# Optimization experiments

Hardware: AMD Instinct MI355X
Metric: run time of the kernel (lower is better)

Reference implementation:

```python
import jax, jax.numpy as jnp
import numpy as np

B, C, F, T = 4, 64, 64, 128
IC = 32  # inter_channels = C // 2
EPS = 1e-5  # BatchNorm eps


def _conv1x1(x, w, b=None):
    # x: (B, Cin, H, W), w: (Cout, Cin)
    y = jnp.einsum('bchw,oc->bohw', x, w)
    if b is not None:
        y = y + b[None, :, None, None]
    return y


def _maxpool2(x):
    b, c, h, w = x.shape
    return x.reshape(b, c, h // 2, 2, w // 2, 2).max(axis=(3, 5))


def _pos_score(fsz, tsz, h2_w):
    # positional encoding is (fpos, tpos) in [0,1]; the 2->1 conv head makes the
    # pos_delta contribution separable: score(n,m) = s(n) - s(m)
    fpos = jnp.linspace(0.0, 1.0, fsz)
    tpos = jnp.linspace(0.0, 1.0, tsz)
    return (h2_w[0] * fpos[:, None] + h2_w[1] * tpos[None, :]).reshape(-1)


def setup_inputs() -> dict:
    key = jax.random.key(0)
    ks = jax.random.split(key, 16)
    s = 0.05
    inp = {
        'x': jax.random.normal(ks[0], (B, C, F, T), dtype=jnp.float32),
        'psi_w': jax.random.normal(ks[1], (IC, C)) * s,
        'psi_b': jax.random.normal(ks[2], (IC,)) * s,
        'theta_w': jax.random.normal(ks[3], (IC, C)) * s,
        'theta_b': jax.random.normal(ks[4], (IC,)) * s,
        'phi_w': jax.random.normal(ks[5], (IC, C)) * s,
        'phi_b': jax.random.normal(ks[6], (IC,)) * s,
        'h0_w': jax.random.normal(ks[7], (IC,)) * s,
        'h1_w': jax.random.normal(ks[8], (IC,)) * s,
        'h2_w': jax.random.normal(ks[9], (2,)) * s,
        'W_w': jax.random.normal(ks[10], (C, IC + 1)) * s,
        'W_b': jax.random.normal(ks[11], (C,)) * s,
        'bn_gamma': jax.random.normal(ks[12], (C,)) * s + 1.0,
        'bn_beta': jax.random.normal(ks[13], (C,)) * s,
        'bn_mean': jax.random.normal(ks[14], (C,)) * s,
        'bn_var': jax.random.uniform(ks[15], (C,), minval=0.5, maxval=1.5),
    }
    return inp


def reference(x, psi_w, psi_b, theta_w, theta_b, phi_w, phi_b,
              h0_w, h1_w, h2_w, W_w, W_b, bn_gamma, bn_beta, bn_mean, bn_var):
    Bs, Cs, Fs, Ts = x.shape
    N = Fs * Ts
    M = (Fs // 2) * (Ts // 2)

    psi_x = _maxpool2(_conv1x1(x, psi_w, psi_b))      # (B, IC, F/2, T/2)
    theta_x = _conv1x1(x, theta_w, theta_b)           # (B, IC, F, T)
    phi_x = _maxpool2(_conv1x1(x, phi_w, phi_b))      # (B, IC, F/2, T/2)

    # additive attention scores: relu(head0(theta) + head1(phi) + head2(pos_delta))
    t_score = jnp.einsum('bcft,c->bft', theta_x, h0_w).reshape(Bs, N)   # (B, N)
    p_score = jnp.einsum('bcft,c->bft', phi_x, h1_w).reshape(Bs, M)     # (B, M)
    a = _pos_score(Fs, Ts, h2_w)             # (N,) query pos contribution
    bpos = _pos_score(Fs // 2, Ts // 2, h2_w)  # (M,) key pos contribution
    f = jax.nn.relu((t_score + a[None, :])[:, :, None]
                    + (p_score - bpos[None, :])[:, None, :])  # (B, N, M)

    f_div = f / jnp.asarray(M, f.dtype)
    psi_flat = psi_x.reshape(Bs, IC, M)
    y = jnp.einsum('bnm,bcm->bcn', f_div, psi_flat).reshape(Bs, IC, Fs, Ts)

    # r_structure_type='zero' -> structure feature is zeros (1 extra channel)
    structure = jnp.zeros((Bs, 1, Fs, Ts), dtype=y.dtype)
    y = jnp.concatenate([y, structure], axis=1)       # (B, IC+1, F, T)

    wy = _conv1x1(y, W_w, W_b)                        # (B, C, F, T)
    inv = bn_gamma / jnp.sqrt(bn_var + EPS)
    wy = wy * inv[None, :, None, None] + (bn_beta - bn_mean * inv)[None, :, None, None]
    return wy + x
```

## Files before the change

### kernel.cpp

```cpp
#include <hip/hip_runtime.h>

#define B_ 4
#define C_ 64
#define F_ 64
#define T_ 128
#define IC_ 32
#define N_ 8192
#define M_ 2048

#define OFF_U      0
#define OFF_PSI2   32768
#define OFF_V      294912
#define OFF_VS     303104
#define OFF_Q01    311296
#define WS_FLOATS  1360384

__device__ __align__(16) float g_ws[WS_FLOATS];
__device__ int g_perm[B_ * M_];

__global__ __launch_bounds__(256) void k1(
    const float* __restrict__ x,
    const float* __restrict__ psi_w, const float* __restrict__ psi_b,
    const float* __restrict__ theta_w, const float* __restrict__ theta_b,
    const float* __restrict__ phi_w, const float* __restrict__ phi_b,
    const float* __restrict__ h0_w, const float* __restrict__ h1_w,
    const float* __restrict__ h2_w)
{
    float* __restrict__ ws = g_ws;
    __shared__ __align__(16) float xs[4096];
    __shared__ __align__(16) float pw[2048];
    __shared__ __align__(16) float fw[2048];
    __shared__ float wt_l[64];

    const int tid = threadIdx.x;
    const int bid = blockIdx.x;
    const int b = bid >> 7;
    const int rem = bid & 127;
    const int fh = rem >> 2;
    const int q = rem & 3;
    const int c0 = q * 32;

    for (int idx = tid; idx < 1024; idx += 256) {
        const int c = idx >> 4, r2 = (idx >> 3) & 1, t4 = idx & 7;
        const float4 v = *(const float4*)&x[(((size_t)b * 64 + c) * 64 + (2 * fh + r2)) * 128 + c0 + 4 * t4];
        *(float4*)&xs[c * 64 + r2 * 32 + 4 * t4] = v;
    }
    for (int idx = tid; idx < 2048; idx += 256) {
        const int c4 = idx >> 7, o = (idx >> 2) & 31, j = idx & 3;
        pw[idx] = psi_w[o * 64 + 4 * c4 + j];
        fw[idx] = phi_w[o * 64 + 4 * c4 + j];
    }
    if (tid < 64) {
        float acc = 0.f;
        for (int o2 = 0; o2 < 32; ++o2)
            acc += h0_w[o2] * theta_w[o2 * 64 + tid];
        wt_l[tid] = acc;
    }
    __syncthreads();

    const float h20 = h2_w[0], h21 = h2_w[1];

    {
        const int o = tid & 31, g = tid >> 5;
        const float pb = psi_b[o], fb = phi_b[o], h1 = h1_w[o];
        const float4* pw4 = (const float4*)pw;
        const float4* fw4 = (const float4*)fw;
        const float4* xs4 = (const float4*)xs;
        float sp[2][4] = {{0,0,0,0},{0,0,0,0}};
        float sf[2][4] = {{0,0,0,0},{0,0,0,0}};
        for (int c4 = 0; c4 < 16; ++c4) {
            const float4 pv = pw4[c4 * 32 + o];
            const float4 fv = fw4[c4 * 32 + o];
            const float* pvf = (const float*)&pv;
            const float* fvf = (const float*)&fv;
#pragma unroll
            for (int j = 0; j < 4; ++j) {
                const int c = 4 * c4 + j;
                const float4 r0 = xs4[c * 16 + g];
                const float4 r1 = xs4[c * 16 + 8 + g];
                const float wp = pvf[j], wf = fvf[j];
                sp[0][0] += wp * r0.x; sp[0][1] += wp * r0.y;
                sp[0][2] += wp * r1.x; sp[0][3] += wp * r1.y;
                sp[1][0] += wp * r0.z; sp[1][1] += wp * r0.w;
                sp[1][2] += wp * r1.z; sp[1][3] += wp * r1.w;
                sf[0][0] += wf * r0.x; sf[0][1] += wf * r0.y;
                sf[0][2] += wf * r1.x; sf[0][3] += wf * r1.y;
                sf[1][0] += wf * r0.z; sf[1][1] += wf * r0.w;
                sf[1][2] += wf * r1.z; sf[1][3] += wf * r1.w;
            }
        }
#pragma unroll
        for (int h = 0; h < 2; ++h) {
            const int hc = 2 * g + h;
            const float psiv = fmaxf(fmaxf(sp[h][0], sp[h][1]), fmaxf(sp[h][2], sp[h][3])) + pb;
            const float phiv = fmaxf(fmaxf(sf[h][0], sf[h][1]), fmaxf(sf[h][2], sf[h][3])) + fb;
            const int m = fh * 64 + q * 16 + hc;
            ws[OFF_PSI2 + ((size_t)b * 2048 + m) * 32 + o] = psiv;
            float tv = h1 * phiv;
            for (int mask = 1; mask < 32; mask <<= 1)
                tv += __shfl_xor(tv, mask, 64);
            if (o == 0) {
                const float bpos = h20 * (fh * (1.0f / 31.0f))
                                 + h21 * ((q * 16 + hc) * (1.0f / 63.0f));
                ws[OFF_V + b * 2048 + m] = tv - bpos;
            }
        }
    }

    if (tid < 64) {
        const int r2 = tid >> 5, tl = tid & 31;
        float acc = 0.f;
        for (int c = 0; c < 64; ++c)
            acc += xs[c * 64 + r2 * 32 + tl] * wt_l[c];
        float tb_ = 0.f;
        for (int o2 = 0; o2 < 32; ++o2)
            tb_ += h0_w[o2] * theta_b[o2];
        const int f = 2 * fh + r2, tt = c0 + tl;
        const int n = f * 128 + tt;
        const float a = h20 * (f * (1.0f / 63.0f)) + h21 * (tt * (1.0f / 127.0f));
        ws[OFF_U + b * 8192 + n] = acc + tb_ + a;
    }
}

__global__ __launch_bounds__(256) void k2()
{
    float* __restrict__ ws = g_ws;
    __shared__ __align__(16) float vl[2048];
    __shared__ int part[256];
    const int tid = threadIdx.x;
    const int b = blockIdx.x >> 7, chunk = blockIdx.x & 127;
    const float* v = ws + OFF_V + b * 2048;
    for (int i = tid; i < 2048; i += 256) vl[i] = v[i];
    __syncthreads();

    const int ml = tid >> 4;
    const int jq = tid & 15;
    const int m = chunk * 16 + ml;
    const float vm = vl[m];
    int cnt = 0;
    const float4* v4 = (const float4*)vl;
#pragma unroll 4
    for (int i = 0; i < 32; ++i) {
        const int j4 = jq + 16 * i;
        const float4 vv = v4[j4];
        const int jb = j4 * 4;
        cnt += (vv.x > vm) || (vv.x == vm && (jb    ) < m);
        cnt += (vv.y > vm) || (vv.y == vm && (jb + 1) < m);
        cnt += (vv.z > vm) || (vv.z == vm && (jb + 2) < m);
        cnt += (vv.w > vm) || (vv.w == vm && (jb + 3) < m);
    }
    part[tid] = cnt;
    __syncthreads();
    if (tid < 16) {
        int r = 0;
#pragma unroll
        for (int j = 0; j < 16; ++j) r += part[tid * 16 + j];
        ws[OFF_VS + b * 2048 + r] = vl[chunk * 16 + tid];
        g_perm[b * 2048 + r] = chunk * 16 + tid;
    }
}

__global__ __launch_bounds__(512) void k3(const float* __restrict__ W_w)
{
    float* __restrict__ ws = g_ws;
    __shared__ float Wrow[32];
    __shared__ float wt0[8], wt1[8];
    const int tid = threadIdx.x;
    const int b = blockIdx.x >> 6, o = blockIdx.x & 63;
    if (tid < 32) Wrow[tid] = W_w[o * 33 + tid];
    __syncthreads();

    const int* perm = g_perm + b * 2048;
    const float* vs = ws + OFF_VS + b * 2048;
    const float* psi2 = ws + OFF_PSI2 + (size_t)b * 2048 * 32;

    float zl[4], vlv[4];
    float s0 = 0.f, s1 = 0.f;
    const int base = tid * 4;
#pragma unroll
    for (int qq = 0; qq < 4; ++qq) {
        const int i = base + qq;
        const int mp = perm[i];
        const float4* pr = (const float4*)(psi2 + (size_t)mp * 32);
        float z = 0.f;
#pragma unroll
        for (int w = 0; w < 8; ++w) {
            const float4 p4 = pr[w];
            z += Wrow[4 * w] * p4.x + Wrow[4 * w + 1] * p4.y
               + Wrow[4 * w + 2] * p4.z + Wrow[4 * w + 3] * p4.w;
        }
        const float vv = vs[i];
        zl[qq] = z; vlv[qq] = vv;
        s0 += z; s1 += vv * z;
    }

    float w0 = s0, w1 = s1;
    const int lane = tid & 63, wv = tid >> 6;
#pragma unroll
    for (int off = 1; off < 64; off <<= 1) {
        const float t0_ = __shfl_up(w0, off, 64);
        const float t1_ = __shfl_up(w1, off, 64);
        if (lane >= off) { w0 += t0_; w1 += t1_; }
    }
    if (lane == 63) { wt0[wv] = w0; wt1[wv] = w1; }
    __syncthreads();
    float base0 = 0.f, base1 = 0.f;
    for (int w = 0; w < wv; ++w) { base0 += wt0[w]; base1 += wt1[w]; }
    float r0 = w0 + base0 - s0, r1 = w1 + base1 - s1;

    float2* Q01 = (float2*)(ws + OFF_Q01) + (size_t)b * 2049 * 64;
#pragma unroll
    for (int qq = 0; qq < 4; ++qq) {
        r0 += zl[qq]; r1 += vlv[qq] * zl[qq];
        float2 p; p.x = r0; p.y = r1;
        Q01[(size_t)(base + qq + 1) * 64 + o] = p;
    }
    if (tid == 0) { float2 z2; z2.x = 0.f; z2.y = 0.f; Q01[o] = z2; }
}

__global__ __launch_bounds__(512) void k4(
    const float* __restrict__ x,
    const float* __restrict__ W_b,
    const float* __restrict__ bn_g, const float* __restrict__ bn_b,
    const float* __restrict__ bn_m, const float* __restrict__ bn_v,
    float* __restrict__ out)
{
    const float* __restrict__ ws = g_ws;
    __shared__ __align__(16) float vsl[2048];
    __shared__ float tileb[64 * 65];
    __shared__ int karr[64];
    __shared__ float uarr[64];

    const int tid = threadIdx.x;
    const int b = blockIdx.x >> 7, tile = blockIdx.x & 127;
    const int n0 = tile * 64;

    const float* vs = ws + OFF_VS + b * 2048;
    for (int i = tid; i < 2048; i += 512) vsl[i] = vs[i];
    __syncthreads();

    if (tid < 64) {
        const float u = ws[OFF_U + b * 8192 + n0 + tid];
        const float thr = -u;
        int lo = 0, hi = 2048;
        while (lo < hi) {
            const int mid = (lo + hi) >> 1;
            if (vsl[mid] > thr) lo = mid + 1; else hi = mid;
        }
        karr[tid] = lo;
        uarr[tid] = u;
    }
    __syncthreads();

    const int lane = tid & 63, w = tid >> 6;
    const float inv = bn_g[lane] * __frsqrt_rn(bn_v[lane] + 1e-5f);
    const float sft = W_b[lane] * inv + bn_b[lane] - bn_m[lane] * inv;
    const float2* Q01 = (const float2*)(ws + OFF_Q01) + (size_t)b * 2049 * 64;

    for (int nl = w; nl < 64; nl += 8) {
        const int k = karr[nl];
        const float u = uarr[nl];
        const float2 qv = Q01[(size_t)k * 64 + lane];
        const float raw = (u * qv.x + qv.y) * (1.0f / 2048.0f);
        tileb[lane * 65 + nl] = raw * inv + sft;
    }
    __syncthreads();

    for (int idx = tid; idx < 2048; idx += 512) {
        const int o = idx >> 5, j2 = idx & 31;
        const size_t gi = ((size_t)b * 64 + o) * 8192 + n0 + 2 * j2;
        const float2 xv = *(const float2*)&x[gi];
        float2 r;
        r.x = tileb[o * 65 + 2 * j2] + xv.x;
        r.y = tileb[o * 65 + 2 * j2 + 1] + xv.y;
        *(float2*)&out[gi] = r;
    }
}

extern "C" void kernel_launch(void* const* d_in, const int* in_sizes, int n_in,
                              void* d_out, int out_size, void* d_ws, size_t ws_size,
                              hipStream_t stream)
{
    (void)in_sizes; (void)n_in; (void)out_size; (void)d_ws; (void)ws_size;
    const float* x       = (const float*)d_in[0];
    const float* psi_w   = (const float*)d_in[1];
    const float* psi_b   = (const float*)d_in[2];
    const float* theta_w = (const float*)d_in[3];
    const float* theta_b = (const float*)d_in[4];
    const float* phi_w   = (const float*)d_in[5];
    const float* phi_b   = (const float*)d_in[6];
    const float* h0_w    = (const float*)d_in[7];
    const float* h1_w    = (const float*)d_in[8];
    const float* h2_w    = (const float*)d_in[9];
    const float* W_w     = (const float*)d_in[10];
    const float* W_b     = (const float*)d_in[11];
    const float* bn_g    = (const float*)d_in[12];
    const float* bn_b    = (const float*)d_in[13];
    const float* bn_m    = (const float*)d_in[14];
    const float* bn_v    = (const float*)d_in[15];
    float* out = (float*)d_out;

    k1<<<dim3(512), dim3(256), 0, stream>>>(x, psi_w, psi_b, theta_w, theta_b,
                                            phi_w, phi_b, h0_w, h1_w, h2_w);
    k2<<<dim3(512), dim3(256), 0, stream>>>();
    k3<<<dim3(256), dim3(512), 0, stream>>>(W_w);
    k4<<<dim3(512), dim3(512), 0, stream>>>(x, W_b, bn_g, bn_b, bn_m, bn_v, out);
}
```

Baseline: 126.8 us.

## Fuse four kernels into one persistent kernel with atomic grid barriers

Replaces the four separate launches with a single 256-block kernel that runs each former stage in turn and separates them with a software grid barrier built on an atomic counter. Each block now handles two work units per stage. The goal is to remove kernel launch gaps and inter-kernel drain time. The cost is barrier spin latency, half the blocks and threads doing each stage's work, and the assumption that all 256 blocks are resident at once.

Result: slower. 307.1 us (+142.2%).

```diff
diff --git a/kernel.cpp b/kernel.cpp
--- a/kernel.cpp
+++ b/kernel.cpp
@@ -17,263 +17,303 @@
 
 __device__ __align__(16) float g_ws[WS_FLOATS];
 __device__ int g_perm[B_ * M_];
-
-__global__ __launch_bounds__(256) void k1(
+__device__ unsigned g_bar;
+
+#define GRID_ 256
+
+__device__ __forceinline__ void grid_barrier(int tid)
+{
+    __threadfence();
+    __syncthreads();
+    if (tid == 0) {
+        const unsigned t = __hip_atomic_fetch_add(&g_bar, 1u, __ATOMIC_ACQ_REL,
+                                                  __HIP_MEMORY_SCOPE_AGENT) + 1u;
+        const unsigned goal = (t + (GRID_ - 1u)) & ~(GRID_ - 1u);
+        while (__hip_atomic_load(&g_bar, __ATOMIC_ACQUIRE,
+                                 __HIP_MEMORY_SCOPE_AGENT) < goal)
+            __builtin_amdgcn_s_sleep(2);
+    }
+    __syncthreads();
+    __threadfence();
+}
+
+__global__ __launch_bounds__(256, 2) void fused(
     const float* __restrict__ x,
     const float* __restrict__ psi_w, const float* __restrict__ psi_b,
     const float* __restrict__ theta_w, const float* __restrict__ theta_b,
     const float* __restrict__ phi_w, const float* __restrict__ phi_b,
     const float* __restrict__ h0_w, const float* __restrict__ h1_w,
-    const float* __restrict__ h2_w)
-{
-    float* __restrict__ ws = g_ws;
-    __shared__ __align__(16) float xs[4096];
-    __shared__ __align__(16) float pw[2048];
-    __shared__ __align__(16) float fw[2048];
-    __shared__ float wt_l[64];
-
-    const int tid = threadIdx.x;
-    const int bid = blockIdx.x;
-    const int b = bid >> 7;
-    const int rem = bid & 127;
-    const int fh = rem >> 2;
-    const int q = rem & 3;
-    const int c0 = q * 32;
-
-    for (int idx = tid; idx < 1024; idx += 256) {
-        const int c = idx >> 4, r2 = (idx >> 3) & 1, t4 = idx & 7;
-        const float4 v = *(const float4*)&x[(((size_t)b * 64 + c) * 64 + (2 * fh + r2)) * 128 + c0 + 4 * t4];
-        *(float4*)&xs[c * 64 + r2 * 32 + 4 * t4] = v;
-    }
-    for (int idx = tid; idx < 2048; idx += 256) {
-        const int c4 = idx >> 7, o = (idx >> 2) & 31, j = idx & 3;
-        pw[idx] = psi_w[o * 64 + 4 * c4 + j];
-        fw[idx] = phi_w[o * 64 + 4 * c4 + j];
-    }
-    if (tid < 64) {
-        float acc = 0.f;
-        for (int o2 = 0; o2 < 32; ++o2)
-            acc += h0_w[o2] * theta_w[o2 * 64 + tid];
-        wt_l[tid] = acc;
-    }
-    __syncthreads();
-
-    const float h20 = h2_w[0], h21 = h2_w[1];
-
-    {
-        const int o = tid & 31, g = tid >> 5;
-        const float pb = psi_b[o], fb = phi_b[o], h1 = h1_w[o];
-        const float4* pw4 = (const float4*)pw;
-        const float4* fw4 = (const float4*)fw;
-        const float4* xs4 = (const float4*)xs;
-        float sp[2][4] = {{0,0,0,0},{0,0,0,0}};
-        float sf[2][4] = {{0,0,0,0},{0,0,0,0}};
-        for (int c4 = 0; c4 < 16; ++c4) {
-            const float4 pv = pw4[c4 * 32 + o];
-            const float4 fv = fw4[c4 * 32 + o];
-            const float* pvf = (const float*)&pv;
-            const float* fvf = (const float*)&fv;
-#pragma unroll
-            for (int j = 0; j < 4; ++j) {
-                const int c = 4 * c4 + j;
-                const float4 r0 = xs4[c * 16 + g];
-                const float4 r1 = xs4[c * 16 + 8 + g];
-                const float wp = pvf[j], wf = fvf[j];
-                sp[0][0] += wp * r0.x; sp[0][1] += wp * r0.y;
-                sp[0][2] += wp * r1.x; sp[0][3] += wp * r1.y;
-                sp[1][0] += wp * r0.z; sp[1][1] += wp * r0.w;
-                sp[1][2] += wp * r1.z; sp[1][3] += wp * r1.w;
-                sf[0][0] += wf * r0.x; sf[0][1] += wf * r0.y;
-                sf[0][2] += wf * r1.x; sf[0][3] += wf * r1.y;
-                sf[1][0] += wf * r0.z; sf[1][1] += wf * r0.w;
-                sf[1][2] += wf * r1.z; sf[1][3] += wf * r1.w;
-            }
-        }
-#pragma unroll
-        for (int h = 0; h < 2; ++h) {
-            const int hc = 2 * g + h;
-            const float psiv = fmaxf(fmaxf(sp[h][0], sp[h][1]), fmaxf(sp[h][2], sp[h][3])) + pb;
-            const float phiv = fmaxf(fmaxf(sf[h][0], sf[h][1]), fmaxf(sf[h][2], sf[h][3])) + fb;
-            const int m = fh * 64 + q * 16 + hc;
-            ws[OFF_PSI2 + ((size_t)b * 2048 + m) * 32 + o] = psiv;
-            float tv = h1 * phiv;
-            for (int mask = 1; mask < 32; mask <<= 1)
-                tv += __shfl_xor(tv, mask, 64);
-            if (o == 0) {
-                const float bpos = h20 * (fh * (1.0f / 31.0f))
-                                 + h21 * ((q * 16 + hc) * (1.0f / 63.0f));
-                ws[OFF_V + b * 2048 + m] = tv - bpos;
-            }
-        }
-    }
-
-    if (tid < 64) {
-        const int r2 = tid >> 5, tl = tid & 31;
-        float acc = 0.f;
-        for (int c = 0; c < 64; ++c)
-            acc += xs[c * 64 + r2 * 32 + tl] * wt_l[c];
-        float tb_ = 0.f;
-        for (int o2 = 0; o2 < 32; ++o2)
-            tb_ += h0_w[o2] * theta_b[o2];
-        const int f = 2 * fh + r2, tt = c0 + tl;
-        const int n = f * 128 + tt;
-        const float a = h20 * (f * (1.0f / 63.0f)) + h21 * (tt * (1.0f / 127.0f));
-        ws[OFF_U + b * 8192 + n] = acc + tb_ + a;
-    }
-}
-
-__global__ __launch_bounds__(256) void k2()
-{
-    float* __restrict__ ws = g_ws;
-    __shared__ __align__(16) float vl[2048];
-    __shared__ int part[256];
-    const int tid = threadIdx.x;
-    const int b = blockIdx.x >> 7, chunk = blockIdx.x & 127;
-    const float* v = ws + OFF_V + b * 2048;
-    for (int i = tid; i < 2048; i += 256) vl[i] = v[i];
-    __syncthreads();
-
-    const int ml = tid >> 4;
-    const int jq = tid & 15;
-    const int m = chunk * 16 + ml;
-    const float vm = vl[m];
-    int cnt = 0;
-    const float4* v4 = (const float4*)vl;
-#pragma unroll 4
-    for (int i = 0; i < 32; ++i) {
-        const int j4 = jq + 16 * i;
-        const float4 vv = v4[j4];
-        const int jb = j4 * 4;
-        cnt += (vv.x > vm) || (vv.x == vm && (jb    ) < m);
-        cnt += (vv.y > vm) || (vv.y == vm && (jb + 1) < m);
-        cnt += (vv.z > vm) || (vv.z == vm && (jb + 2) < m);
-        cnt += (vv.w > vm) || (vv.w == vm && (jb + 3) < m);
-    }
-    part[tid] = cnt;
-    __syncthreads();
-    if (tid < 16) {
-        int r = 0;
-#pragma unroll
-        for (int j = 0; j < 16; ++j) r += part[tid * 16 + j];
-        ws[OFF_VS + b * 2048 + r] = vl[chunk * 16 + tid];
-        g_perm[b * 2048 + r] = chunk * 16 + tid;
-    }
-}
-
-__global__ __launch_bounds__(512) void k3(const float* __restrict__ W_w)
-{
-    float* __restrict__ ws = g_ws;
-    __shared__ float Wrow[32];
-    __shared__ float wt0[8], wt1[8];
-    const int tid = threadIdx.x;
-    const int b = blockIdx.x >> 6, o = blockIdx.x & 63;
-    if (tid < 32) Wrow[tid] = W_w[o * 33 + tid];
-    __syncthreads();
-
-    const int* perm = g_perm + b * 2048;
-    const float* vs = ws + OFF_VS + b * 2048;
-    const float* psi2 = ws + OFF_PSI2 + (size_t)b * 2048 * 32;
-
-    float zl[4], vlv[4];
-    float s0 = 0.f, s1 = 0.f;
-    const int base = tid * 4;
-#pragma unroll
-    for (int qq = 0; qq < 4; ++qq) {
-        const int i = base + qq;
-        const int mp = perm[i];
-        const float4* pr = (const float4*)(psi2 + (size_t)mp * 32);
-        float z = 0.f;
-#pragma unroll
-        for (int w = 0; w < 8; ++w) {
-            const float4 p4 = pr[w];
-            z += Wrow[4 * w] * p4.x + Wrow[4 * w + 1] * p4.y
-               + Wrow[4 * w + 2] * p4.z + Wrow[4 * w + 3] * p4.w;
-        }
-        const float vv = vs[i];
-        zl[qq] = z; vlv[qq] = vv;
-        s0 += z; s1 += vv * z;
-    }
-
-    float w0 = s0, w1 = s1;
-    const int lane = tid & 63, wv = tid >> 6;
-#pragma unroll
-    for (int off = 1; off < 64; off <<= 1) {
-        const float t0_ = __shfl_up(w0, off, 64);
-        const float t1_ = __shfl_up(w1, off, 64);
-        if (lane >= off) { w0 += t0_; w1 += t1_; }
-    }
-    if (lane == 63) { wt0[wv] = w0; wt1[wv] = w1; }
-    __syncthreads();
-    float base0 = 0.f, base1 = 0.f;
-    for (int w = 0; w < wv; ++w) { base0 += wt0[w]; base1 += wt1[w]; }
-    float r0 = w0 + base0 - s0, r1 = w1 + base1 - s1;
-
-    float2* Q01 = (float2*)(ws + OFF_Q01) + (size_t)b * 2049 * 64;
-#pragma unroll
-    for (int qq = 0; qq < 4; ++qq) {
-        r0 += zl[qq]; r1 += vlv[qq] * zl[qq];
-        float2 p; p.x = r0; p.y = r1;
-        Q01[(size_t)(base + qq + 1) * 64 + o] = p;
-    }
-    if (tid == 0) { float2 z2; z2.x = 0.f; z2.y = 0.f; Q01[o] = z2; }
-}
-
-__global__ __launch_bounds__(512) void k4(
-    const float* __restrict__ x,
-    const float* __restrict__ W_b,
+    const float* __restrict__ h2_w,
+    const float* __restrict__ W_w, const float* __restrict__ W_b,
     const float* __restrict__ bn_g, const float* __restrict__ bn_b,
     const float* __restrict__ bn_m, const float* __restrict__ bn_v,
     float* __restrict__ out)
 {
-    const float* __restrict__ ws = g_ws;
-    __shared__ __align__(16) float vsl[2048];
-    __shared__ float tileb[64 * 65];
-    __shared__ int karr[64];
-    __shared__ float uarr[64];
+    float* __restrict__ ws = g_ws;
+    __shared__ __align__(16) char smem[33024];
 
     const int tid = threadIdx.x;
-    const int b = blockIdx.x >> 7, tile = blockIdx.x & 127;
-    const int n0 = tile * 64;
-
-    const float* vs = ws + OFF_VS + b * 2048;
-    for (int i = tid; i < 2048; i += 512) vsl[i] = vs[i];
-    __syncthreads();
-
-    if (tid < 64) {
-        const float u = ws[OFF_U + b * 8192 + n0 + tid];
-        const float thr = -u;
-        int lo = 0, hi = 2048;
-        while (lo < hi) {
-            const int mid = (lo + hi) >> 1;
-            if (vsl[mid] > thr) lo = mid + 1; else hi = mid;
-        }
-        karr[tid] = lo;
-        uarr[tid] = u;
-    }
-    __syncthreads();
-
-    const int lane = tid & 63, w = tid >> 6;
-    const float inv = bn_g[lane] * __frsqrt_rn(bn_v[lane] + 1e-5f);
-    const float sft = W_b[lane] * inv + bn_b[lane] - bn_m[lane] * inv;
-    const float2* Q01 = (const float2*)(ws + OFF_Q01) + (size_t)b * 2049 * 64;
-
-    for (int nl = w; nl < 64; nl += 8) {
-        const int k = karr[nl];
-        const float u = uarr[nl];
-        const float2 qv = Q01[(size_t)k * 64 + lane];
-        const float raw = (u * qv.x + qv.y) * (1.0f / 2048.0f);
-        tileb[lane * 65 + nl] = raw * inv + sft;
-    }
-    __syncthreads();
-
-    for (int idx = tid; idx < 2048; idx += 512) {
-        const int o = idx >> 5, j2 = idx & 31;
-        const size_t gi = ((size_t)b * 64 + o) * 8192 + n0 + 2 * j2;
-        const float2 xv = *(const float2*)&x[gi];
-        float2 r;
-        r.x = tileb[o * 65 + 2 * j2] + xv.x;
-        r.y = tileb[o * 65 + 2 * j2 + 1] + xv.y;
-        *(float2*)&out[gi] = r;
+    const int bid = blockIdx.x;
+
+    {
+        float* xs   = (float*)smem;
+        float* pw   = xs + 4096;
+        float* fw   = pw + 2048;
+        float* wt_l = fw + 2048;
+
+        for (int idx = tid; idx < 2048; idx += 256) {
+            const int c4 = idx >> 7, o = (idx >> 2) & 31, j = idx & 3;
+            pw[idx] = psi_w[o * 64 + 4 * c4 + j];
+            fw[idx] = phi_w[o * 64 + 4 * c4 + j];
+        }
+        if (tid < 64) {
+            float acc = 0.f;
+            for (int o2 = 0; o2 < 32; ++o2)
+                acc += h0_w[o2] * theta_w[o2 * 64 + tid];
+            wt_l[tid] = acc;
+        }
+
+        const float h20 = h2_w[0], h21 = h2_w[1];
+
+        for (int half = 0; half < 2; ++half) {
+            const int u = 2 * bid + half;
+            const int b = u >> 7;
+            const int rem = u & 127;
+            const int fh = rem >> 2;
+            const int q = rem & 3;
+            const int c0 = q * 32;
+
+            __syncthreads();
+
+            for (int idx = tid; idx < 1024; idx += 256) {
+                const int c = idx >> 4, r2 = (idx >> 3) & 1, t4 = idx & 7;
+                const float4 v = *(const float4*)&x[(((size_t)b * 64 + c) * 64 + (2 * fh + r2)) * 128 + c0 + 4 * t4];
+                *(float4*)&xs[c * 64 + r2 * 32 + 4 * t4] = v;
+            }
+            __syncthreads();
+
+            {
+                const int o = tid & 31, g = tid >> 5;
+                const float pb = psi_b[o], fb = phi_b[o], h1 = h1_w[o];
+                const float4* pw4 = (const float4*)pw;
+                const float4* fw4 = (const float4*)fw;
+                const float4* xs4 = (const float4*)xs;
+                float sp[2][4] = {{0,0,0,0},{0,0,0,0}};
+                float sf[2][4] = {{0,0,0,0},{0,0,0,0}};
+                for (int c4 = 0; c4 < 16; ++c4) {
+                    const float4 pv = pw4[c4 * 32 + o];
+                    const float4 fv = fw4[c4 * 32 + o];
+                    const float* pvf = (const float*)&pv;
+                    const float* fvf = (const float*)&fv;
+#pragma unroll
+                    for (int j = 0; j < 4; ++j) {
+                        const int c = 4 * c4 + j;
+                        const float4 r0 = xs4[c * 16 + g];
+                        const float4 r1 = xs4[c * 16 + 8 + g];
+                        const float wp = pvf[j], wf = fvf[j];
+                        sp[0][0] += wp * r0.x; sp[0][1] += wp * r0.y;
+                        sp[0][2] += wp * r1.x; sp[0][3] += wp * r1.y;
+                        sp[1][0] += wp * r0.z; sp[1][1] += wp * r0.w;
+                        sp[1][2] += wp * r1.z; sp[1][3] += wp * r1.w;
+                        sf[0][0] += wf * r0.x; sf[0][1] += wf * r0.y;
+                        sf[0][2] += wf * r1.x; sf[0][3] += wf * r1.y;
+                        sf[1][0] += wf * r0.z; sf[1][1] += wf * r0.w;
+                        sf[1][2] += wf * r1.z; sf[1][3] += wf * r1.w;
+                    }
+                }
+#pragma unroll
+                for (int h = 0; h < 2; ++h) {
+                    const int hc = 2 * g + h;
+                    const float psiv = fmaxf(fmaxf(sp[h][0], sp[h][1]), fmaxf(sp[h][2], sp[h][3])) + pb;
+                    const float phiv = fmaxf(fmaxf(sf[h][0], sf[h][1]), fmaxf(sf[h][2], sf[h][3])) + fb;
+                    const int m = fh * 64 + q * 16 + hc;
+                    ws[OFF_PSI2 + ((size_t)b * 2048 + m) * 32 + o] = psiv;
+                    float tv = h1 * phiv;
+                    for (int mask = 1; mask < 32; mask <<= 1)
+                        tv += __shfl_xor(tv, mask, 64);
+                    if (o == 0) {
+                        const float bpos = h20 * (fh * (1.0f / 31.0f))
+                                         + h21 * ((q * 16 + hc) * (1.0f / 63.0f));
+                        ws[OFF_V + b * 2048 + m] = tv - bpos;
+                    }
+                }
+            }
+
+            if (tid < 64) {
+                const int r2 = tid >> 5, tl = tid & 31;
+                float acc = 0.f;
+                for (int c = 0; c < 64; ++c)
+                    acc += xs[c * 64 + r2 * 32 + tl] * wt_l[c];
+                float tb_ = 0.f;
+                for (int o2 = 0; o2 < 32; ++o2)
+                    tb_ += h0_w[o2] * theta_b[o2];
+                const int f = 2 * fh + r2, tt = c0 + tl;
+                const int n = f * 128 + tt;
+                const float a = h20 * (f * (1.0f / 63.0f)) + h21 * (tt * (1.0f / 127.0f));
+                ws[OFF_U + b * 8192 + n] = acc + tb_ + a;
+            }
+        }
+    }
+
+    grid_barrier(tid);
+
+    {
+        float* vl = (float*)smem;
+        int* part = (int*)(vl + 2048);
+
+        const int u0 = 2 * bid;
+        const int b = u0 >> 7;
+        const float* v = ws + OFF_V + b * 2048;
+        for (int i = tid; i < 2048; i += 256) vl[i] = v[i];
+        __syncthreads();
+
+        const float4* v4 = (const float4*)vl;
+        for (int half = 0; half < 2; ++half) {
+            const int chunk = (u0 & 127) + half;
+            const int ml = tid >> 4;
+            const int jq = tid & 15;
+            const int m = chunk * 16 + ml;
+            const float vm = vl[m];
+            int cnt = 0;
+#pragma unroll 4
+            for (int i = 0; i < 32; ++i) {
+                const int j4 = jq + 16 * i;
+                const float4 vv = v4[j4];
+                const int jb = j4 * 4;
+                cnt += (vv.x > vm) || (vv.x == vm && (jb    ) < m);
+                cnt += (vv.y > vm) || (vv.y == vm && (jb + 1) < m);
+                cnt += (vv.z > vm) || (vv.z == vm && (jb + 2) < m);
+                cnt += (vv.w > vm) || (vv.w == vm && (jb + 3) < m);
+            }
+            part[tid] = cnt;
+            __syncthreads();
+            if (tid < 16) {
+                int r = 0;
+#pragma unroll
+                for (int j = 0; j < 16; ++j) r += part[tid * 16 + j];
+                ws[OFF_VS + b * 2048 + r] = vl[chunk * 16 + tid];
+                g_perm[b * 2048 + r] = chunk * 16 + tid;
+            }
+            __syncthreads();
+        }
+    }
+
+    grid_barrier(tid);
+
+    {
+        float* Wrow = (float*)smem;
+        float* wt0  = Wrow + 32;
+        float* wt1  = wt0 + 4;
+
+        const int b = bid >> 6, o = bid & 63;
+        if (tid < 32) Wrow[tid] = W_w[o * 33 + tid];
+        __syncthreads();
+
+        const int* perm = g_perm + b * 2048;
+        const float* vs = ws + OFF_VS + b * 2048;
+        const float* psi2 = ws + OFF_PSI2 + (size_t)b * 2048 * 32;
+
+        float zl[8], vlv[8];
+        float s0 = 0.f, s1 = 0.f;
+        const int base = tid * 8;
+#pragma unroll
+        for (int qq = 0; qq < 8; ++qq) {
+            const int i = base + qq;
+            const int mp = perm[i];
+            const float4* pr = (const float4*)(psi2 + (size_t)mp * 32);
+            float z = 0.f;
+#pragma unroll
+            for (int w = 0; w < 8; ++w) {
+                const float4 p4 = pr[w];
+                z += Wrow[4 * w] * p4.x + Wrow[4 * w + 1] * p4.y
+                   + Wrow[4 * w + 2] * p4.z + Wrow[4 * w + 3] * p4.w;
+            }
+            const float vv = vs[i];
+            zl[qq] = z; vlv[qq] = vv;
+            s0 += z; s1 += vv * z;
+        }
+
+        float w0 = s0, w1 = s1;
+        const int lane = tid & 63, wv = tid >> 6;
+#pragma unroll
+        for (int off = 1; off < 64; off <<= 1) {
+            const float t0_ = __shfl_up(w0, off, 64);
+            const float t1_ = __shfl_up(w1, off, 64);
+            if (lane >= off) { w0 += t0_; w1 += t1_; }
+        }
+        if (lane == 63) { wt0[wv] = w0; wt1[wv] = w1; }
+        __syncthreads();
+        float base0 = 0.f, base1 = 0.f;
+        for (int w = 0; w < wv; ++w) { base0 += wt0[w]; base1 += wt1[w]; }
+        float r0 = w0 + base0 - s0, r1 = w1 + base1 - s1;
+
+        float2* Q01 = (float2*)(ws + OFF_Q01) + (size_t)b * 2049 * 64;
+#pragma unroll
+        for (int qq = 0; qq < 8; ++qq) {
+            r0 += zl[qq]; r1 += vlv[qq] * zl[qq];
+            float2 p; p.x = r0; p.y = r1;
+            Q01[(size_t)(base + qq + 1) * 64 + o] = p;
+        }
+        if (tid == 0) { float2 z2; z2.x = 0.f; z2.y = 0.f; Q01[o] = z2; }
+    }
+
+    grid_barrier(tid);
+
+    {
+        float* vsl   = (float*)smem;
+        float* tileb = vsl + 2048;
+        float* uarr  = tileb + 4160;
+        int*   karr  = (int*)(uarr + 64);
+
+        const int u0 = 2 * bid;
+        const int b = u0 >> 7;
+
+        const float* vs = ws + OFF_VS + b * 2048;
+        for (int i = tid; i < 2048; i += 256) vsl[i] = vs[i];
+
+        const int lane = tid & 63, w = tid >> 6;
+        const float inv = bn_g[lane] * __frsqrt_rn(bn_v[lane] + 1e-5f);
+        const float sft = W_b[lane] * inv + bn_b[lane] - bn_m[lane] * inv;
+        const float2* Q01 = (const float2*)(ws + OFF_Q01) + (size_t)b * 2049 * 64;
+        __syncthreads();
+
+        for (int half = 0; half < 2; ++half) {
+            const int tile = (u0 & 127) + half;
+            const int n0 = tile * 64;
+
+            if (tid < 64) {
+                const float u = ws[OFF_U + b * 8192 + n0 + tid];
+                const float thr = -u;
+                int lo = 0, hi = 2048;
+                while (lo < hi) {
+                    const int mid = (lo + hi) >> 1;
+                    if (vsl[mid] > thr) lo = mid + 1; else hi = mid;
+                }
+                karr[tid] = lo;
+                uarr[tid] = u;
+            }
+            __syncthreads();
+
+            for (int nl = w; nl < 64; nl += 4) {
+                const int k = karr[nl];
+                const float u = uarr[nl];
+                const float2 qv = Q01[(size_t)k * 64 + lane];
+                const float raw = (u * qv.x + qv.y) * (1.0f / 2048.0f);
+                tileb[lane * 65 + nl] = raw * inv + sft;
+            }
+            __syncthreads();
+
+            for (int idx = tid; idx < 2048; idx += 256) {
+                const int o = idx >> 5, j2 = idx & 31;
+                const size_t gi = ((size_t)b * 64 + o) * 8192 + n0 + 2 * j2;
+                const float2 xv = *(const float2*)&x[gi];
+                float2 r;
+                r.x = tileb[o * 65 + 2 * j2] + xv.x;
+                r.y = tileb[o * 65 + 2 * j2 + 1] + xv.y;
+                *(float2*)&out[gi] = r;
+            }
+            __syncthreads();
+        }
     }
 }
 
@@ -300,9 +340,7 @@
     const float* bn_v    = (const float*)d_in[15];
     float* out = (float*)d_out;
 
-    k1<<<dim3(512), dim3(256), 0, stream>>>(x, psi_w, psi_b, theta_w, theta_b,
-                                            phi_w, phi_b, h0_w, h1_w, h2_w);
-    k2<<<dim3(512), dim3(256), 0, stream>>>();
-    k3<<<dim3(256), dim3(512), 0, stream>>>(W_w);
-    k4<<<dim3(512), dim3(512), 0, stream>>>(x, W_b, bn_g, bn_b, bn_m, bn_v, out);
+    fused<<<dim3(GRID_), dim3(256), 0, stream>>>(
+        x, psi_w, psi_b, theta_w, theta_b, phi_w, phi_b,
+        h0_w, h1_w, h2_w, W_w, W_b, bn_g, bn_b, bn_m, bn_v, out);
 }
```

## Precompute W·psi projections in k1 and gather scalar z in k3

Applied to the files above, without the earlier changes.

k1 now projects each pooled psi vector through all 64 rows of W_w and stores a 64-wide z per key position, replacing the stored 32-wide psi. k3 then gathers one scalar per permuted key instead of re-reading 32 psi values and redoing the dot product for each of the 64 output channels. The workspace doubles for this buffer and k1 takes on extra shared memory and arithmetic. k4 also loads the sorted v array with one float4 per thread instead of a strided loop.

Result: faster. 120.2 us (-5.2%).

```diff
diff --git a/kernel.cpp b/kernel.cpp
--- a/kernel.cpp
+++ b/kernel.cpp
@@ -9,11 +9,11 @@
 #define M_ 2048
 
 #define OFF_U      0
-#define OFF_PSI2   32768
-#define OFF_V      294912
-#define OFF_VS     303104
-#define OFF_Q01    311296
-#define WS_FLOATS  1360384
+#define OFF_Z      32768
+#define OFF_V      557056
+#define OFF_VS     565248
+#define OFF_Q01    573440
+#define WS_FLOATS  1622528
 
 __device__ __align__(16) float g_ws[WS_FLOATS];
 __device__ int g_perm[B_ * M_];
@@ -24,12 +24,14 @@
     const float* __restrict__ theta_w, const float* __restrict__ theta_b,
     const float* __restrict__ phi_w, const float* __restrict__ phi_b,
     const float* __restrict__ h0_w, const float* __restrict__ h1_w,
-    const float* __restrict__ h2_w)
+    const float* __restrict__ h2_w, const float* __restrict__ W_w)
 {
     float* __restrict__ ws = g_ws;
     __shared__ __align__(16) float xs[4096];
     __shared__ __align__(16) float pw[2048];
     __shared__ __align__(16) float fw[2048];
+    __shared__ __align__(16) float Wl[2048];
+    __shared__ __align__(16) float pt[512];
     __shared__ float wt_l[64];
 
     const int tid = threadIdx.x;
@@ -49,6 +51,8 @@
         const int c4 = idx >> 7, o = (idx >> 2) & 31, j = idx & 3;
         pw[idx] = psi_w[o * 64 + 4 * c4 + j];
         fw[idx] = phi_w[o * 64 + 4 * c4 + j];
+        const int c4w = idx >> 8, o64 = (idx >> 2) & 63, jw = idx & 3;
+        Wl[idx] = W_w[o64 * 33 + 4 * c4w + jw];
     }
     if (tid < 64) {
         float acc = 0.f;
@@ -95,7 +99,7 @@
             const float psiv = fmaxf(fmaxf(sp[h][0], sp[h][1]), fmaxf(sp[h][2], sp[h][3])) + pb;
             const float phiv = fmaxf(fmaxf(sf[h][0], sf[h][1]), fmaxf(sf[h][2], sf[h][3])) + fb;
             const int m = fh * 64 + q * 16 + hc;
-            ws[OFF_PSI2 + ((size_t)b * 2048 + m) * 32 + o] = psiv;
+            pt[hc * 32 + o] = psiv;
             float tv = h1 * phiv;
             for (int mask = 1; mask < 32; mask <<= 1)
                 tv += __shfl_xor(tv, mask, 64);
@@ -104,6 +108,30 @@
                                  + h21 * ((q * 16 + hc) * (1.0f / 63.0f));
                 ws[OFF_V + b * 2048 + m] = tv - bpos;
             }
+        }
+    }
+    __syncthreads();
+
+    {
+        const int op = tid & 63, mseg = tid >> 6;
+        const float4* Wl4 = (const float4*)Wl;
+        const float4* pt4 = (const float4*)pt;
+        float4 wreg[8];
+#pragma unroll
+        for (int c4 = 0; c4 < 8; ++c4)
+            wreg[c4] = Wl4[c4 * 64 + op];
+#pragma unroll
+        for (int j = 0; j < 4; ++j) {
+            const int ml = mseg * 4 + j;
+            float acc = 0.f;
+#pragma unroll
+            for (int c4 = 0; c4 < 8; ++c4) {
+                const float4 pv = pt4[ml * 8 + c4];
+                acc += wreg[c4].x * pv.x + wreg[c4].y * pv.y
+                     + wreg[c4].z * pv.z + wreg[c4].w * pv.w;
+            }
+            const int m = fh * 64 + q * 16 + ml;
+            ws[OFF_Z + ((size_t)b * 2048 + m) * 64 + op] = acc;
         }
     }
 
@@ -160,19 +188,16 @@
     }
 }
 
-__global__ __launch_bounds__(512) void k3(const float* __restrict__ W_w)
+__global__ __launch_bounds__(512) void k3()
 {
     float* __restrict__ ws = g_ws;
-    __shared__ float Wrow[32];
     __shared__ float wt0[8], wt1[8];
     const int tid = threadIdx.x;
     const int b = blockIdx.x >> 6, o = blockIdx.x & 63;
-    if (tid < 32) Wrow[tid] = W_w[o * 33 + tid];
-    __syncthreads();
 
     const int* perm = g_perm + b * 2048;
     const float* vs = ws + OFF_VS + b * 2048;
-    const float* psi2 = ws + OFF_PSI2 + (size_t)b * 2048 * 32;
+    const float* zg = ws + OFF_Z + (size_t)b * 2048 * 64 + o;
 
     float zl[4], vlv[4];
     float s0 = 0.f, s1 = 0.f;
@@ -181,14 +206,7 @@
     for (int qq = 0; qq < 4; ++qq) {
         const int i = base + qq;
         const int mp = perm[i];
-        const float4* pr = (const float4*)(psi2 + (size_t)mp * 32);
-        float z = 0.f;
-#pragma unroll
-        for (int w = 0; w < 8; ++w) {
-            const float4 p4 = pr[w];
-            z += Wrow[4 * w] * p4.x + Wrow[4 * w + 1] * p4.y
-               + Wrow[4 * w + 2] * p4.z + Wrow[4 * w + 3] * p4.w;
-        }
+        const float z = zg[(size_t)mp * 64];
         const float vv = vs[i];
         zl[qq] = z; vlv[qq] = vv;
         s0 += z; s1 += vv * z;
@@ -236,7 +254,7 @@
     const int n0 = tile * 64;
 
     const float* vs = ws + OFF_VS + b * 2048;
-    for (int i = tid; i < 2048; i += 512) vsl[i] = vs[i];
+    *(float4*)&vsl[tid * 4] = *(const float4*)&vs[tid * 4];
     __syncthreads();
 
     if (tid < 64) {
@@ -301,8 +319,8 @@
     float* out = (float*)d_out;
 
     k1<<<dim3(512), dim3(256), 0, stream>>>(x, psi_w, psi_b, theta_w, theta_b,
-                                            phi_w, phi_b, h0_w, h1_w, h2_w);
+                                            phi_w, phi_b, h0_w, h1_w, h2_w, W_w);
     k2<<<dim3(512), dim3(256), 0, stream>>>();
-    k3<<<dim3(256), dim3(512), 0, stream>>>(W_w);
+    k3<<<dim3(256), dim3(512), 0, stream>>>();
     k4<<<dim3(512), dim3(512), 0, stream>>>(x, W_b, bn_g, bn_b, bn_m, bn_v, out);
 }
```
